# Optimization experiments

Hardware: AMD Instinct MI355X
Metric: run time of the kernel (lower is better)

The kernel has to match this reference:

```python
import jax, jax.numpy as jnp
import numpy as np

N_NODES = 50000
N_EDGES = 400000
C = 32            # channels per irrep (scalars and l=1 vectors)
N_BASIS = 8
HID = 64          # radial MLP hidden dim
N_LAYERS = 2
N_SPECIES = 86
N_GRAPHS = 64
R_MAX = 5.0
EPS = 1e-5


def setup_inputs() -> dict:
    key = jax.random.key(0)
    ks = jax.random.split(key, 16)
    species = jax.random.randint(ks[0], (N_NODES,), 0, N_SPECIES)
    pos = jax.random.normal(ks[1], (N_NODES, 3), jnp.float32)
    edge_index = jax.random.randint(ks[2], (2, N_EDGES), 0, N_NODES)
    batch = jnp.sort(jax.random.randint(ks[3], (N_NODES,), 0, N_GRAPHS))

    emb = jax.random.normal(ks[4], (N_SPECIES, C), jnp.float32) * 0.1
    freqs = jnp.arange(1, N_BASIS + 1, dtype=jnp.float32) * jnp.pi / R_MAX  # trainable Bessel freqs
    rW1 = jax.random.normal(ks[5], (N_LAYERS, N_BASIS, HID), jnp.float32) / np.sqrt(N_BASIS)
    rb1 = jnp.zeros((N_LAYERS, HID), jnp.float32)
    rW2 = jax.random.normal(ks[6], (N_LAYERS, HID, HID), jnp.float32) / np.sqrt(HID)
    rb2 = jnp.zeros((N_LAYERS, HID), jnp.float32)
    rW3 = jax.random.normal(ks[7], (N_LAYERS, HID, 4 * C), jnp.float32) / np.sqrt(HID)
    rb3 = jnp.zeros((N_LAYERS, 4 * C), jnp.float32)
    Wss = jax.random.normal(ks[8], (N_LAYERS, C, C), jnp.float32) / np.sqrt(C)
    bss = jnp.zeros((N_LAYERS, C), jnp.float32)
    Wvv = jax.random.normal(ks[9], (N_LAYERS, C, C), jnp.float32) / np.sqrt(C)
    bn_gs = jnp.ones((N_LAYERS, C), jnp.float32)
    bn_bs = jnp.zeros((N_LAYERS, C), jnp.float32)
    bn_gv = jnp.ones((N_LAYERS, C), jnp.float32)
    W_out = jax.random.normal(ks[10], (C, 1), jnp.float32) / np.sqrt(C)
    b_out = jnp.zeros((1,), jnp.float32)
    atom_ref = jnp.zeros((N_SPECIES, 1), jnp.float32)  # AtomRef init zeros
    return dict(species=species, pos=pos, edge_index=edge_index, batch=batch,
                emb=emb, freqs=freqs, rW1=rW1, rb1=rb1, rW2=rW2, rb2=rb2,
                rW3=rW3, rb3=rb3, Wss=Wss, bss=bss, Wvv=Wvv,
                bn_gs=bn_gs, bn_bs=bn_bs, bn_gv=bn_gv,
                W_out=W_out, b_out=b_out, atom_ref=atom_ref)


def _bessel_basis(dist, freqs):
    # basis = sin(f*r)/r with smooth polynomial cutoff (as in BesselRadialBasis.forward)
    d = jnp.clip(dist, 0.0)
    basis = jnp.sin(freqs[None, :] * d[:, None]) / jnp.clip(d, 1e-6)[:, None]
    x = jnp.clip(d / R_MAX, 0.0, 1.0)
    cut = 1.0 - 6.0 * x ** 5 + 15.0 * x ** 4 - 10.0 * x ** 3
    cut = jnp.where(d <= R_MAX, cut, 0.0)
    return basis * cut[:, None]


def _forward(species, pos, edge_index, batch, emb, freqs, rW1, rb1, rW2, rb2,
             rW3, rb3, Wss, bss, Wvv, bn_gs, bn_bs, bn_gv, W_out, b_out, atom_ref):
    src, dst = edge_index[0], edge_index[1]
    vec = pos[dst] - pos[src]                      # (E,3) edge vectors
    dist = jnp.sqrt(jnp.sum(vec * vec, axis=-1))   # (E,)
    basis = _bessel_basis(dist, freqs)             # (E,NB)
    Y1 = vec / jnp.clip(dist, 1e-9)[:, None]       # (E,3) l=1 spherical harmonics (unit dir)

    s = emb[species]                               # (N,C) scalar features
    v = jnp.zeros((s.shape[0], C, 3), s.dtype)     # (N,C,3) l=1 features

    for l in range(N_LAYERS):
        # radial MLP -> per-edge channel-wise tensor-product weights (4 paths x C)
        h = jax.nn.silu(basis @ rW1[l] + rb1[l])
        h = jax.nn.silu(h @ rW2[l] + rb2[l])
        w = h @ rW3[l] + rb3[l]                    # (E,4C)
        w1, w2, w3, w4 = jnp.split(w, 4, axis=-1)  # each (E,C)

        xs = s[src]                                # (E,C)   gather
        xv = v[src]                                # (E,C,3) gather
        # TP paths: s*Y0 -> scalar; (v.Y1) -> gate scalar; s*Y1 -> vector; v*Y0 -> vector
        m_sf = w1 * xs                                               # (E,C)
        m_sg = w2 * jnp.einsum('ecd,ed->ec', xv, Y1)                 # (E,C)
        m_v = w3[..., None] * xs[..., None] * Y1[:, None, :] + w4[..., None] * xv  # (E,C,3)

        agg_sf = jax.ops.segment_sum(m_sf, dst, num_segments=N_NODES)
        agg_sg = jax.ops.segment_sum(m_sg, dst, num_segments=N_NODES)
        agg_v = jax.ops.segment_sum(m_v, dst, num_segments=N_NODES)

        # gated nonlinearity: silu on scalars, sigmoid gate on vectors
        s_new = jax.nn.silu(agg_sf)
        v_new = jax.nn.sigmoid(agg_sg)[..., None] * agg_v

        # self-interaction (equivariant linear mixing over channels)
        s_new = s_new @ Wss[l] + bss[l]
        v_new = jnp.einsum('ncd,cm->nmd', v_new, Wvv[l])

        # e3nn-style batch norm: standardize scalars; norm-normalize vectors
        mu = jnp.mean(s_new, axis=0)
        var = jnp.mean((s_new - mu) ** 2, axis=0)
        s_new = (s_new - mu) / jnp.sqrt(var + EPS) * bn_gs[l] + bn_bs[l]
        vnorm2 = jnp.mean(jnp.sum(v_new * v_new, axis=-1), axis=0) / 3.0  # per-channel, /(2l+1)
        v_new = v_new / jnp.sqrt(vnorm2 + EPS)[None, :, None] * bn_gv[l][None, :, None]

        # residual (irreps match)
        s = s + s_new
        v = v + v_new

    node_e = s @ W_out + b_out                                       # (N,1)
    graph_e = jax.ops.segment_sum(node_e, batch, num_segments=N_GRAPHS)
    ref_e = jax.ops.segment_sum(atom_ref[species], batch, num_segments=N_GRAPHS)
    return graph_e + ref_e                                           # (B,1)


def reference(species, pos, edge_index, batch, emb, freqs, rW1, rb1, rW2, rb2,
              rW3, rb3, Wss, bss, Wvv, bn_gs, bn_bs, bn_gv, W_out, b_out, atom_ref):
    return _forward(species, pos, edge_index, batch, emb, freqs, rW1, rb1, rW2, rb2,
                    rW3, rb3, Wss, bss, Wvv, bn_gs, bn_bs, bn_gv, W_out, b_out, atom_ref)
```

## Files before the change

### kernel.cpp

```cpp
#include <hip/hip_runtime.h>
#include <math.h>

#define N_NODES 50000
#define N_EDGES 400000
#define C 32
#define NB 8
#define HID 64
#define NL 2
#define NG 64
#define RMAXF 5.0f
#define EPSF 1e-5f
#define TBL 4096
#define BN_BLOCKS 512
#define NBLK_N ((N_NODES + 255) / 256)

__device__ __forceinline__ float silu_f(float x) { return x / (1.0f + __expf(-x)); }
__device__ __forceinline__ float sigmoid_f(float x) { return 1.0f / (1.0f + __expf(-x)); }
__device__ __forceinline__ void atomAddF(float* p, float val) {
  __hip_atomic_fetch_add(p, val, __ATOMIC_RELAXED, __HIP_MEMORY_SCOPE_AGENT);
}
__device__ __forceinline__ void atomAddD(double* p, double val) {
  __hip_atomic_fetch_add(p, val, __ATOMIC_RELAXED, __HIP_MEMORY_SCOPE_AGENT);
}
__device__ __forceinline__ unsigned short bf16_rne(float f) {
  unsigned u = __float_as_uint(f);
  return (unsigned short)((u + 0x7FFFu + ((u >> 16) & 1u)) >> 16);
}
__device__ __forceinline__ float bfu(unsigned short u) {
  return __uint_as_float(((unsigned)u) << 16);
}

__global__ __launch_bounds__(256) void k_edge_geom(
    const float* __restrict__ pos, const int* __restrict__ ei,
    const float* __restrict__ freqs,
    float* __restrict__ basis, float* __restrict__ Y1)
{
  int e = blockIdx.x * 256 + threadIdx.x;
  if (e >= N_EDGES) return;
  int s = ei[e], d = ei[N_EDGES + e];
  float vx = pos[d*3+0] - pos[s*3+0];
  float vy = pos[d*3+1] - pos[s*3+1];
  float vz = pos[d*3+2] - pos[s*3+2];
  float dist = sqrtf(vx*vx + vy*vy + vz*vz);
  float invd = 1.0f / fmaxf(dist, 1e-9f);
  Y1[e*3+0] = vx*invd; Y1[e*3+1] = vy*invd; Y1[e*3+2] = vz*invd;
  float x = fminf(fmaxf(dist * (1.0f/RMAXF), 0.0f), 1.0f);
  float x2 = x*x, x3 = x2*x;
  float cut = 1.0f - x3 * (10.0f - 15.0f*x + 6.0f*x2);
  if (dist > RMAXF) cut = 0.0f;
  float rinv = cut / fmaxf(dist, 1e-6f);
  #pragma unroll
  for (int k = 0; k < NB; k++)
    basis[e*NB + k] = sinf(freqs[k] * dist) * rinv;
}

__global__ __launch_bounds__(256) void k_node_init(
    const int* __restrict__ species, const float* __restrict__ emb,
    float* __restrict__ s, unsigned short* __restrict__ s_bf)
{
  int i = blockIdx.x * 256 + threadIdx.x;
  if (i >= N_NODES * C) return;
  int n = i >> 5, c = i & 31;
  float x = emb[species[n]*C + c];
  s[i] = x;
  s_bf[i] = bf16_rne(x);
}

__global__ __launch_bounds__(256) void k_hist(const int* __restrict__ ei, int* __restrict__ counts)
{
  int e = blockIdx.x * 256 + threadIdx.x;
  if (e >= N_EDGES) return;
  atomicAdd(&counts[ei[N_EDGES + e]], 1);
}

__global__ __launch_bounds__(256) void k_scanA(const int* __restrict__ counts, int* __restrict__ bsum)
{
  __shared__ int sh[256];
  int i = blockIdx.x * 256 + threadIdx.x;
  int x = (i < N_NODES) ? counts[i] : 0;
  sh[threadIdx.x] = x;
  __syncthreads();
  for (int off = 128; off > 0; off >>= 1) {
    if (threadIdx.x < off) sh[threadIdx.x] += sh[threadIdx.x + off];
    __syncthreads();
  }
  if (threadIdx.x == 0) bsum[blockIdx.x] = sh[0];
}

__global__ __launch_bounds__(256) void k_scanB(int* __restrict__ bsum)
{
  __shared__ int sh[256];
  int tid = threadIdx.x;
  int x = (tid < NBLK_N) ? bsum[tid] : 0;
  sh[tid] = x;
  __syncthreads();
  for (int off = 1; off < 256; off <<= 1) {
    int y = (tid >= off) ? sh[tid - off] : 0;
    __syncthreads();
    sh[tid] += y;
    __syncthreads();
  }
  if (tid < NBLK_N) bsum[tid] = sh[tid] - x;
}

__global__ __launch_bounds__(256) void k_scanC(const int* __restrict__ counts,
                                               const int* __restrict__ bsum,
                                               int* __restrict__ row_start)
{
  __shared__ int sh[256];
  int i = blockIdx.x * 256 + threadIdx.x;
  int x = (i < N_NODES) ? counts[i] : 0;
  sh[threadIdx.x] = x;
  __syncthreads();
  for (int off = 1; off < 256; off <<= 1) {
    int y = (threadIdx.x >= off) ? sh[threadIdx.x - off] : 0;
    __syncthreads();
    sh[threadIdx.x] += y;
    __syncthreads();
  }
  if (i < N_NODES) row_start[i] = bsum[blockIdx.x] + sh[threadIdx.x] - x;
}

__global__ __launch_bounds__(256) void k_geom_scatter(
    const float* __restrict__ pos, const int* __restrict__ ei,
    const int* __restrict__ row_start, int* __restrict__ cursor,
    int* __restrict__ srcs, float* __restrict__ Y1s, float* __restrict__ dist_s)
{
  int e = blockIdx.x * 256 + threadIdx.x;
  if (e >= N_EDGES) return;
  int s = ei[e], d = ei[N_EDGES + e];
  float vx = pos[d*3+0] - pos[s*3+0];
  float vy = pos[d*3+1] - pos[s*3+1];
  float vz = pos[d*3+2] - pos[s*3+2];
  float dist = sqrtf(vx*vx + vy*vy + vz*vz);
  float invd = 1.0f / fmaxf(dist, 1e-9f);
  int p = row_start[d] + atomicAdd(&cursor[d], 1);
  srcs[p] = s;
  dist_s[p] = dist;
  Y1s[p*3+0] = vx*invd;
  Y1s[p*3+1] = vy*invd;
  Y1s[p*3+2] = vz*invd;
}

__global__ __launch_bounds__(256) void k_table_h(
    const float* __restrict__ freqs,
    const float* __restrict__ rW1, const float* __restrict__ rb1,
    const float* __restrict__ rW2, const float* __restrict__ rb2,
    float* __restrict__ h2tab)
{
  int idx = blockIdx.x * 256 + threadIdx.x;
  if (idx >= NL * TBL) return;
  int l = idx / TBL, i = idx - l * TBL;
  float d = (float)i * (RMAXF / (float)(TBL - 1));
  float x = fminf(fmaxf(d * (1.0f/RMAXF), 0.0f), 1.0f);
  float x2 = x*x, x3 = x2*x;
  float cut = 1.0f - x3 * (10.0f - 15.0f*x + 6.0f*x2);
  float rinv = cut / fmaxf(d, 1e-6f);
  float bas[NB];
  #pragma unroll
  for (int k = 0; k < NB; k++) bas[k] = sinf(freqs[k] * d) * rinv;

  const float* W1 = rW1 + l*NB*HID;
  const float* B1 = rb1 + l*HID;
  const float* W2 = rW2 + l*HID*HID;
  const float* B2 = rb2 + l*HID;

  float h2[HID];
  #pragma unroll
  for (int j = 0; j < HID; j++) h2[j] = B2[j];
  #pragma unroll 2
  for (int k = 0; k < HID; k++) {
    float t = B1[k];
    #pragma unroll
    for (int b = 0; b < NB; b++) t = fmaf(bas[b], W1[b*HID + k], t);
    float h1k = silu_f(t);
    const float* r = W2 + k*HID;
    #pragma unroll
    for (int j = 0; j < HID; j++) h2[j] = fmaf(h1k, r[j], h2[j]);
  }
  float* out = h2tab + (size_t)idx * HID;
  #pragma unroll
  for (int j = 0; j < HID; j++) out[j] = silu_f(h2[j]);
}

__global__ __launch_bounds__(256) void k_table_w(
    const float* __restrict__ h2tab,
    const float* __restrict__ rW3, const float* __restrict__ rb3,
    float* __restrict__ wtab)
{
  int idx = blockIdx.x * 256 + threadIdx.x;
  if (idx >= NL * TBL * 16) return;
  int chunk = idx & 15;
  int row   = idx >> 4;
  int l     = row / TBL;
  const float* h2 = h2tab + (size_t)row * HID;
  const float* W3 = rW3 + l*HID*4*C + chunk*8;
  const float* B3 = rb3 + l*4*C + chunk*8;
  float a[8];
  #pragma unroll
  for (int ci = 0; ci < 8; ci++) a[ci] = B3[ci];
  #pragma unroll 4
  for (int k = 0; k < HID; k++) {
    float h = h2[k];
    #pragma unroll
    for (int ci = 0; ci < 8; ci++) a[ci] = fmaf(h, W3[k*4*C + ci], a[ci]);
  }
  float* out = wtab + (size_t)row * 128 + chunk*8;
  #pragma unroll
  for (int ci = 0; ci < 8; ci++) out[ci] = a[ci];
}

__global__ __launch_bounds__(256) void k_agg_update(
    const float* __restrict__ tb,
    const float* __restrict__ dist_s, const float* __restrict__ Y1s,
    const int* __restrict__ srcs,
    const int* __restrict__ row_start, const int* __restrict__ counts,
    const unsigned short* __restrict__ s_bf, const unsigned short* __restrict__ v_bf,
    const float* __restrict__ Wss, const float* __restrict__ bss,
    const float* __restrict__ Wvv,
    float* __restrict__ s_new, float* __restrict__ v_new)
{
  int t = blockIdx.x * 256 + threadIdx.x;
  int n = t >> 5;
  int c = t & 31;

  const float SCALE = (float)(TBL - 1) / RMAXF;
  float asf = 0.0f, asg = 0.0f, av0 = 0.0f, av1 = 0.0f, av2 = 0.0f;
  int beg = row_start[n], cnt = counts[n];

  int i = 0;
  for (; i + 1 < cnt; i += 2) {
    int pA = beg + i, pB = beg + i + 1;
    float dA = dist_s[pA],  dB = dist_s[pB];
    int srcA = srcs[pA],    srcB = srcs[pB];
    float yA0 = Y1s[pA*3+0], yA1 = Y1s[pA*3+1], yA2 = Y1s[pA*3+2];
    float yB0 = Y1s[pB*3+0], yB1 = Y1s[pB*3+1], yB2 = Y1s[pB*3+2];

    float tsA = fminf(dA, RMAXF) * SCALE;
    int t0A = (int)tsA; t0A = t0A > TBL-2 ? TBL-2 : t0A;
    float frA = tsA - (float)t0A;
    float tsB = fminf(dB, RMAXF) * SCALE;
    int t0B = (int)tsB; t0B = t0B > TBL-2 ? TBL-2 : t0B;
    float frB = tsB - (float)t0B;

    const float* rA0 = tb + (size_t)t0A * 128 + c;
    const float* rA1 = rA0 + 128;
    const float* rB0 = tb + (size_t)t0B * 128 + c;
    const float* rB1 = rB0 + 128;

    float a00 = rA0[0],  a01 = rA1[0];
    float a10 = rA0[32], a11 = rA1[32];
    float a20 = rA0[64], a21 = rA1[64];
    float a30 = rA0[96], a31 = rA1[96];
    float b00 = rB0[0],  b01 = rB1[0];
    float b10 = rB0[32], b11 = rB1[32];
    float b20 = rB0[64], b21 = rB1[64];
    float b30 = rB0[96], b31 = rB1[96];

    float xsA = bfu(s_bf[srcA*C + c]);
    const unsigned short* vpA = v_bf + (size_t)(srcA*C + c)*3;
    float xvA0 = bfu(vpA[0]), xvA1 = bfu(vpA[1]), xvA2 = bfu(vpA[2]);
    float xsB = bfu(s_bf[srcB*C + c]);
    const unsigned short* vpB = v_bf + (size_t)(srcB*C + c)*3;
    float xvB0 = bfu(vpB[0]), xvB1 = bfu(vpB[1]), xvB2 = bfu(vpB[2]);

    float w1A = fmaf(frA, a01-a00, a00);
    float w2A = fmaf(frA, a11-a10, a10);
    float w3A = fmaf(frA, a21-a20, a20);
    float w4A = fmaf(frA, a31-a30, a30);
    asf = fmaf(w1A, xsA, asf);
    asg = fmaf(w2A, xvA0*yA0 + xvA1*yA1 + xvA2*yA2, asg);
    float w3xsA = w3A * xsA;
    av0 += fmaf(w3xsA, yA0, w4A*xvA0);
    av1 += fmaf(w3xsA, yA1, w4A*xvA1);
    av2 += fmaf(w3xsA, yA2, w4A*xvA2);

    float w1B = fmaf(frB, b01-b00, b00);
    float w2B = fmaf(frB, b11-b10, b10);
    float w3B = fmaf(frB, b21-b20, b20);
    float w4B = fmaf(frB, b31-b30, b30);
    asf = fmaf(w1B, xsB, asf);
    asg = fmaf(w2B, xvB0*yB0 + xvB1*yB1 + xvB2*yB2, asg);
    float w3xsB = w3B * xsB;
    av0 += fmaf(w3xsB, yB0, w4B*xvB0);
    av1 += fmaf(w3xsB, yB1, w4B*xvB1);
    av2 += fmaf(w3xsB, yB2, w4B*xvB2);
  }
  if (i < cnt) {
    int p = beg + i;
    float d  = dist_s[p];
    int src = srcs[p];
    float y0 = Y1s[p*3+0], y1 = Y1s[p*3+1], y2 = Y1s[p*3+2];
    float ts = fminf(d, RMAXF) * SCALE;
    int   t0 = (int)ts; t0 = t0 > TBL-2 ? TBL-2 : t0;
    float fr = ts - (float)t0;
    const float* r0 = tb + (size_t)t0 * 128 + c;
    const float* r1 = r0 + 128;
    float w1 = fmaf(fr, r1[0]  - r0[0],  r0[0]);
    float w2 = fmaf(fr, r1[32] - r0[32], r0[32]);
    float w3 = fmaf(fr, r1[64] - r0[64], r0[64]);
    float w4 = fmaf(fr, r1[96] - r0[96], r0[96]);
    float xs = bfu(s_bf[src*C + c]);
    const unsigned short* vp = v_bf + (size_t)(src*C + c)*3;
    float xv0 = bfu(vp[0]), xv1 = bfu(vp[1]), xv2 = bfu(vp[2]);
    asf = fmaf(w1, xs, asf);
    asg = fmaf(w2, xv0*y0 + xv1*y1 + xv2*y2, asg);
    float w3xs = w3 * xs;
    av0 += fmaf(w3xs, y0, w4*xv0);
    av1 += fmaf(w3xs, y1, w4*xv1);
    av2 += fmaf(w3xs, y2, w4*xv2);
  }

  float sgv  = silu_f(asf);
  float gate = sigmoid_f(asg);
  float vg0 = gate*av0, vg1 = gate*av1, vg2 = gate*av2;

  float sn = bss[c];
  float vm0 = 0.0f, vm1 = 0.0f, vm2 = 0.0f;
  #pragma unroll
  for (int k = 0; k < C; k++) {
    float a  = __shfl(sgv, k, 32);
    sn = fmaf(a, Wss[k*C + c], sn);
    float wv = Wvv[k*C + c];
    vm0 = fmaf(__shfl(vg0, k, 32), wv, vm0);
    vm1 = fmaf(__shfl(vg1, k, 32), wv, vm1);
    vm2 = fmaf(__shfl(vg2, k, 32), wv, vm2);
  }

  s_new[n*C + c] = sn;
  float* vo = v_new + (size_t)(n*C + c)*3;
  vo[0] = vm0; vo[1] = vm1; vo[2] = vm2;
}

__global__ __launch_bounds__(256) void k_bn_stats(
    const float* __restrict__ s_new, const float* __restrict__ v_new,
    double* __restrict__ bn_sums)
{
  __shared__ float lacc[3*C];
  if (threadIdx.x < 3*C) lacc[threadIdx.x] = 0.0f;
  __syncthreads();
  int c = threadIdx.x & 31;
  float r1 = 0.0f, r2 = 0.0f, r3 = 0.0f;
  const int NC = N_NODES * C;
  for (int i = blockIdx.x * 256 + threadIdx.x; i < NC; i += BN_BLOCKS * 256) {
    float sn = s_new[i];
    const float* vp = v_new + (size_t)i * 3;
    r1 += sn;
    r2 += sn * sn;
    r3 += vp[0]*vp[0] + vp[1]*vp[1] + vp[2]*vp[2];
  }
  atomicAdd(&lacc[c],       r1);
  atomicAdd(&lacc[C + c],   r2);
  atomicAdd(&lacc[2*C + c], r3);
  __syncthreads();
  if (threadIdx.x < 3*C) atomAddD(&bn_sums[threadIdx.x], (double)lacc[threadIdx.x]);
}

__global__ __launch_bounds__(256) void k_apply(
    const float* __restrict__ s_new, const float* __restrict__ v_new,
    const double* __restrict__ bn_sums,
    const float* __restrict__ gs, const float* __restrict__ gv,
    const float* __restrict__ bn_bs,
    float* __restrict__ s, float* __restrict__ v,
    unsigned short* __restrict__ s_bf, unsigned short* __restrict__ v_bf)
{
  int i = blockIdx.x * 256 + threadIdx.x;
  if (i >= N_NODES * C) return;
  int c = i & 31;
  double S1 = bn_sums[c], S2 = bn_sums[C + c], VN = bn_sums[2*C + c];
  float mu  = (float)(S1 / (double)N_NODES);
  float var = (float)(S2 / (double)N_NODES) - mu*mu;
  float vn2 = (float)(VN / (3.0 * (double)N_NODES));
  float ssc = gs[c] / sqrtf(var + EPSF);
  float vsc = gv[c] / sqrtf(vn2 + EPSF);

  float sv = s[i] + (s_new[i] - mu) * ssc + bn_bs[c];
  s[i] = sv;
  s_bf[i] = bf16_rne(sv);
  float* vp = v + (size_t)i*3;
  const float* vn = v_new + (size_t)i*3;
  unsigned short* vb = v_bf + (size_t)i*3;
  #pragma unroll
  for (int d = 0; d < 3; d++) {
    float vv = vp[d] + vn[d] * vsc;
    vp[d] = vv;
    vb[d] = bf16_rne(vv);
  }
}

__global__ __launch_bounds__(256) void k_readout(
    const float* __restrict__ s, const int* __restrict__ species,
    const int* __restrict__ batch,
    const float* __restrict__ W_out, const float* __restrict__ b_out,
    const float* __restrict__ atom_ref, float* __restrict__ out)
{
  __shared__ float acc[NG];
  if (threadIdx.x < NG) acc[threadIdx.x] = 0.0f;
  __syncthreads();
  int n = blockIdx.x * 256 + threadIdx.x;
  if (n < N_NODES) {
    float e = b_out[0] + atom_ref[species[n]];
    #pragma unroll
    for (int c = 0; c < C; c++) e = fmaf(s[n*C + c], W_out[c], e);
    atomicAdd(&acc[batch[n]], e);
  }
  __syncthreads();
  if (threadIdx.x < NG) {
    float a = acc[threadIdx.x];
    if (a != 0.0f) atomAddF(&out[threadIdx.x], a);
  }
}

__global__ __launch_bounds__(256) void k_edge_msg_fb(
    const float* __restrict__ basis, const float* __restrict__ Y1,
    const int* __restrict__ ei,
    const float* __restrict__ s, const float* __restrict__ v,
    const float* __restrict__ rW1, const float* __restrict__ rb1,
    const float* __restrict__ rW2, const float* __restrict__ rb2,
    const float* __restrict__ rW3, const float* __restrict__ rb3,
    float* __restrict__ agg_sf, float* __restrict__ agg_sg, float* __restrict__ agg_v)
{
  int e = blockIdx.x * 256 + threadIdx.x;
  if (e >= N_EDGES) return;
  int src = ei[e], dst = ei[N_EDGES + e];
  const float4 b0 = *(const float4*)(basis + (size_t)e*NB);
  const float4 b1 = *(const float4*)(basis + (size_t)e*NB + 4);
  float bas[NB] = {b0.x, b0.y, b0.z, b0.w, b1.x, b1.y, b1.z, b1.w};
  float h2[HID];
  #pragma unroll
  for (int j = 0; j < HID; j++) h2[j] = rb2[j];
  #pragma unroll 2
  for (int k = 0; k < HID; k++) {
    float t = rb1[k];
    #pragma unroll
    for (int b = 0; b < NB; b++) t = fmaf(bas[b], rW1[b*HID + k], t);
    float h1k = silu_f(t);
    const float* r = rW2 + k*HID;
    #pragma unroll
    for (int j = 0; j < HID; j++) h2[j] = fmaf(h1k, r[j], h2[j]);
  }
  #pragma unroll
  for (int j = 0; j < HID; j++) h2[j] = silu_f(h2[j]);
  float y0 = Y1[e*3+0], y1 = Y1[e*3+1], y2 = Y1[e*3+2];
  #pragma unroll 1
  for (int cb = 0; cb < 16; cb++) {
    float a[8];
    #pragma unroll
    for (int ci = 0; ci < 8; ci++) a[ci] = rb3[cb*8 + ci];
    #pragma unroll
    for (int k = 0; k < HID; k++) {
      float h = h2[k];
      #pragma unroll
      for (int ci = 0; ci < 8; ci++) a[ci] = fmaf(h, rW3[k*4*C + cb*8 + ci], a[ci]);
    }
    #pragma unroll
    for (int ci = 0; ci < 8; ci++) {
      int o = cb*8 + ci;
      int path = o >> 5;
      int c = o & 31;
      float xs = s[src*C + c];
      const float* vp = v + (size_t)(src*C + c)*3;
      float xv0 = vp[0], xv1 = vp[1], xv2 = vp[2];
      if (path == 0) {
        atomAddF(&agg_sf[dst*C + c], a[ci] * xs);
      } else if (path == 1) {
        atomAddF(&agg_sg[dst*C + c], a[ci] * (xv0*y0 + xv1*y1 + xv2*y2));
      } else if (path == 2) {
        float w3xs = a[ci] * xs;
        float* ap = agg_v + (size_t)(dst*C + c)*3;
        atomAddF(ap+0, w3xs*y0); atomAddF(ap+1, w3xs*y1); atomAddF(ap+2, w3xs*y2);
      } else {
        float* ap = agg_v + (size_t)(dst*C + c)*3;
        atomAddF(ap+0, a[ci]*xv0); atomAddF(ap+1, a[ci]*xv1); atomAddF(ap+2, a[ci]*xv2);
      }
    }
  }
}

__global__ __launch_bounds__(256) void k_node_update_fb(
    const float* __restrict__ agg_sf, const float* __restrict__ agg_sg,
    const float* __restrict__ agg_v,
    const float* __restrict__ Wss, const float* __restrict__ bss,
    const float* __restrict__ Wvv,
    float* __restrict__ s_new, float* __restrict__ v_new,
    double* __restrict__ bn_sums)
{
  __shared__ float lacc[3*C];
  int t = blockIdx.x * 256 + threadIdx.x;
  int n = t >> 5;
  int c = t & 31;
  if (threadIdx.x < 3*C) lacc[threadIdx.x] = 0.0f;
  __syncthreads();
  float asf = agg_sf[n*C + c];
  float asg = agg_sg[n*C + c];
  const float* ap = agg_v + (size_t)(n*C + c)*3;
  float av0 = ap[0], av1 = ap[1], av2 = ap[2];
  float sgv = silu_f(asf);
  float gate = sigmoid_f(asg);
  float vg0 = gate*av0, vg1 = gate*av1, vg2 = gate*av2;
  float sn = bss[c];
  float vm0 = 0.0f, vm1 = 0.0f, vm2 = 0.0f;
  #pragma unroll
  for (int k = 0; k < C; k++) {
    float a  = __shfl(sgv, k, 32);
    sn = fmaf(a, Wss[k*C + c], sn);
    float wv = Wvv[k*C + c];
    vm0 = fmaf(__shfl(vg0, k, 32), wv, vm0);
    vm1 = fmaf(__shfl(vg1, k, 32), wv, vm1);
    vm2 = fmaf(__shfl(vg2, k, 32), wv, vm2);
  }
  s_new[n*C + c] = sn;
  float* vo = v_new + (size_t)(n*C + c)*3;
  vo[0] = vm0; vo[1] = vm1; vo[2] = vm2;
  float vn2 = vm0*vm0 + vm1*vm1 + vm2*vm2;
  atomicAdd(&lacc[c], sn);
  atomicAdd(&lacc[C + c], sn*sn);
  atomicAdd(&lacc[2*C + c], vn2);
  __syncthreads();
  if (threadIdx.x < 3*C) atomAddD(&bn_sums[threadIdx.x], (double)lacc[threadIdx.x]);
}

__global__ void k_bn_scales_fb(const double* __restrict__ bn_sums,
                               const float* __restrict__ gs, const float* __restrict__ gv,
                               float* __restrict__ scales)
{
  int m = threadIdx.x;
  if (m >= C) return;
  double S1 = bn_sums[m], S2 = bn_sums[C + m], VN = bn_sums[2*C + m];
  double mu  = S1 / (double)N_NODES;
  double var = S2 / (double)N_NODES - mu*mu;
  double vn2 = VN / (3.0 * (double)N_NODES);
  scales[m]       = (float)mu;
  scales[C + m]   = gs[m] / sqrtf((float)var + EPSF);
  scales[2*C + m] = gv[m] / sqrtf((float)vn2 + EPSF);
}

__global__ __launch_bounds__(256) void k_apply_fb(
    const float* __restrict__ s_new, const float* __restrict__ v_new,
    const float* __restrict__ scales, const float* __restrict__ bn_bs,
    float* __restrict__ s, float* __restrict__ v)
{
  int i = blockIdx.x * 256 + threadIdx.x;
  if (i >= N_NODES * C) return;
  int c = i & 31;
  s[i] += (s_new[i] - scales[c]) * scales[C + c] + bn_bs[c];
  float vs = scales[2*C + c];
  v[(size_t)i*3+0] += v_new[(size_t)i*3+0] * vs;
  v[(size_t)i*3+1] += v_new[(size_t)i*3+1] * vs;
  v[(size_t)i*3+2] += v_new[(size_t)i*3+2] * vs;
}

extern "C" void kernel_launch(void* const* d_in, const int* in_sizes, int n_in,
                              void* d_out, int out_size, void* d_ws, size_t ws_size,
                              hipStream_t stream)
{
  const int*   species  = (const int*)  d_in[0];
  const float* pos      = (const float*)d_in[1];
  const int*   ei       = (const int*)  d_in[2];
  const int*   batch    = (const int*)  d_in[3];
  const float* emb      = (const float*)d_in[4];
  const float* freqs    = (const float*)d_in[5];
  const float* rW1      = (const float*)d_in[6];
  const float* rb1      = (const float*)d_in[7];
  const float* rW2      = (const float*)d_in[8];
  const float* rb2      = (const float*)d_in[9];
  const float* rW3      = (const float*)d_in[10];
  const float* rb3      = (const float*)d_in[11];
  const float* Wss      = (const float*)d_in[12];
  const float* bss      = (const float*)d_in[13];
  const float* Wvv      = (const float*)d_in[14];
  const float* bn_gs    = (const float*)d_in[15];
  const float* bn_bs    = (const float*)d_in[16];
  const float* bn_gv    = (const float*)d_in[17];
  const float* W_out    = (const float*)d_in[18];
  const float* b_out    = (const float*)d_in[19];
  const float* atom_ref = (const float*)d_in[20];

  float* ws = (float*)d_ws;
  size_t off = 0;
  float* basis  = ws + off; off += (size_t)N_EDGES * NB;
  float* Y1     = ws + off; off += (size_t)N_EDGES * 3;
  float* s      = ws + off; off += (size_t)N_NODES * C;
  float* v      = ws + off; off += (size_t)N_NODES * C * 3;
  float* s_new  = ws + off; off += (size_t)N_NODES * C;
  float* v_new  = ws + off; off += (size_t)N_NODES * C * 3;
  double* bn_sums = (double*)(ws + off); off += 192;
  float* scales = ws + off; off += 96;

  size_t ra = off;
  float* Y1s      = ws + ra;            ra += (size_t)N_EDGES * 3;
  float* dist_s   = ws + ra;            ra += (size_t)N_EDGES;
  int*   srcs     = (int*)(ws + ra);    ra += N_EDGES;
  int*   counts   = (int*)(ws + ra);    ra += N_NODES;
  int*   row_start= (int*)(ws + ra);    ra += N_NODES;
  int*   cursor   = (int*)(ws + ra);    ra += N_NODES;
  int*   bsum     = (int*)(ws + ra);    ra += 256;
  float* h2tab    = ws + ra;            ra += (size_t)NL * TBL * HID;
  float* wtab     = ws + ra;            ra += (size_t)NL * TBL * 128;
  unsigned short* s_bf = (unsigned short*)(ws + ra); ra += (size_t)N_NODES * C / 2;
  unsigned short* v_bf = (unsigned short*)(ws + ra); ra += (size_t)N_NODES * C * 3 / 2;
  size_t req_sorted = ra * 4;

  size_t rb = off;
  float* agg_sf = ws + rb; rb += (size_t)N_NODES * C;
  float* agg_sg = ws + rb; rb += (size_t)N_NODES * C;
  float* agg_v  = ws + rb; rb += (size_t)N_NODES * C * 3;

  dim3 b256(256);
  const int gE  = (N_EDGES + 255) / 256;
  const int gNC = (N_NODES * C + 255) / 256;
  const int gN  = (N_NODES + 255) / 256;

  hipMemsetAsync(v, 0, (size_t)N_NODES * C * 3 * sizeof(float), stream);

  if (ws_size >= req_sorted) {
    hipMemsetAsync(v_bf, 0, (size_t)N_NODES * C * 3 * sizeof(unsigned short), stream);
    hipMemsetAsync(counts, 0, N_NODES * sizeof(int), stream);
    hipMemsetAsync(cursor, 0, N_NODES * sizeof(int), stream);
    k_node_init<<<gNC, b256, 0, stream>>>(species, emb, s, s_bf);
    k_hist<<<gE, b256, 0, stream>>>(ei, counts);
    k_scanA<<<NBLK_N, b256, 0, stream>>>(counts, bsum);
    k_scanB<<<1, b256, 0, stream>>>(bsum);
    k_scanC<<<NBLK_N, b256, 0, stream>>>(counts, bsum, row_start);
    k_geom_scatter<<<gE, b256, 0, stream>>>(pos, ei, row_start, cursor,
                                            srcs, Y1s, dist_s);
    k_table_h<<<(NL*TBL)/256, b256, 0, stream>>>(freqs, rW1, rb1, rW2, rb2, h2tab);
    k_table_w<<<(NL*TBL*16)/256, b256, 0, stream>>>(h2tab, rW3, rb3, wtab);

    for (int l = 0; l < NL; l++) {
      hipMemsetAsync(bn_sums, 0, 96 * sizeof(double), stream);
      k_agg_update<<<(N_NODES*C)/256, b256, 0, stream>>>(
          wtab + (size_t)l * TBL * 128, dist_s, Y1s, srcs,
          row_start, counts, s_bf, v_bf, Wss + l*C*C, bss + l*C, Wvv + l*C*C,
          s_new, v_new);
      k_bn_stats<<<BN_BLOCKS, b256, 0, stream>>>(s_new, v_new, bn_sums);
      k_apply<<<gNC, b256, 0, stream>>>(s_new, v_new, bn_sums,
          bn_gs + l*C, bn_gv + l*C, bn_bs + l*C, s, v, s_bf, v_bf);
    }
  } else {
    k_node_init<<<gNC, b256, 0, stream>>>(species, emb, s, (unsigned short*)(ws + off));
    k_edge_geom<<<gE, b256, 0, stream>>>(pos, ei, freqs, basis, Y1);
    for (int l = 0; l < NL; l++) {
      hipMemsetAsync(agg_sf, 0, (size_t)N_NODES * 5 * C * sizeof(float), stream);
      hipMemsetAsync(bn_sums, 0, 96 * sizeof(double), stream);
      k_edge_msg_fb<<<gE, b256, 0, stream>>>(basis, Y1, ei, s, v,
          rW1 + l*NB*HID, rb1 + l*HID, rW2 + l*HID*HID, rb2 + l*HID,
          rW3 + l*HID*4*C, rb3 + l*4*C, agg_sf, agg_sg, agg_v);
      k_node_update_fb<<<(N_NODES*C)/256, b256, 0, stream>>>(agg_sf, agg_sg, agg_v,
          Wss + l*C*C, bss + l*C, Wvv + l*C*C, s_new, v_new, bn_sums);
      k_bn_scales_fb<<<1, 64, 0, stream>>>(bn_sums, bn_gs + l*C, bn_gv + l*C, scales);
      k_apply_fb<<<gNC, b256, 0, stream>>>(s_new, v_new, scales, bn_bs + l*C, s, v);
    }
  }

  hipMemsetAsync(d_out, 0, NG * sizeof(float), stream);
  k_readout<<<gN, b256, 0, stream>>>(s, species, batch, W_out, b_out, atom_ref, (float*)d_out);
}
```

Measured before the change: 332.5 us.

## Pack per-edge records into 32-byte AoS and software-prefetch next edge pair

Replaces the separate sorted arrays for source index, distance and unit vector with one 8-float record per edge, written with a float4 plus one scalar store. The aggregation loop reads each record with a vector load and prefetches the next pair of records one iteration ahead. The odd tail is handled by clamping the index and zeroing the weights, which removes the separate remainder block. The aim is fewer scattered loads and better latency hiding on the gather path. In exchange the record buffer grows, since 3 of the 8 floats per edge are padding.

```diff
diff --git a/kernel.cpp b/kernel.cpp
--- a/kernel.cpp
+++ b/kernel.cpp
@@ -124,7 +124,7 @@
 __global__ __launch_bounds__(256) void k_geom_scatter(
     const float* __restrict__ pos, const int* __restrict__ ei,
     const int* __restrict__ row_start, int* __restrict__ cursor,
-    int* __restrict__ srcs, float* __restrict__ Y1s, float* __restrict__ dist_s)
+    float* __restrict__ rec)
 {
   int e = blockIdx.x * 256 + threadIdx.x;
   if (e >= N_EDGES) return;
@@ -135,11 +135,10 @@
   float dist = sqrtf(vx*vx + vy*vy + vz*vz);
   float invd = 1.0f / fmaxf(dist, 1e-9f);
   int p = row_start[d] + atomicAdd(&cursor[d], 1);
-  srcs[p] = s;
-  dist_s[p] = dist;
-  Y1s[p*3+0] = vx*invd;
-  Y1s[p*3+1] = vy*invd;
-  Y1s[p*3+2] = vz*invd;
+  float* rp = rec + (size_t)p * 8;
+  float4 r0; r0.x = dist; r0.y = __int_as_float(s); r0.z = vx*invd; r0.w = vy*invd;
+  *(float4*)rp = r0;
+  rp[4] = vz*invd;
 }
 
 __global__ __launch_bounds__(256) void k_table_h(
@@ -212,8 +211,7 @@
 
 __global__ __launch_bounds__(256) void k_agg_update(
     const float* __restrict__ tb,
-    const float* __restrict__ dist_s, const float* __restrict__ Y1s,
-    const int* __restrict__ srcs,
+    const float* __restrict__ rec,
     const int* __restrict__ row_start, const int* __restrict__ counts,
     const unsigned short* __restrict__ s_bf, const unsigned short* __restrict__ v_bf,
     const float* __restrict__ Wss, const float* __restrict__ bss,
@@ -228,87 +226,72 @@
   float asf = 0.0f, asg = 0.0f, av0 = 0.0f, av1 = 0.0f, av2 = 0.0f;
   int beg = row_start[n], cnt = counts[n];
 
-  int i = 0;
-  for (; i + 1 < cnt; i += 2) {
-    int pA = beg + i, pB = beg + i + 1;
-    float dA = dist_s[pA],  dB = dist_s[pB];
-    int srcA = srcs[pA],    srcB = srcs[pB];
-    float yA0 = Y1s[pA*3+0], yA1 = Y1s[pA*3+1], yA2 = Y1s[pA*3+2];
-    float yB0 = Y1s[pB*3+0], yB1 = Y1s[pB*3+1], yB2 = Y1s[pB*3+2];
-
-    float tsA = fminf(dA, RMAXF) * SCALE;
-    int t0A = (int)tsA; t0A = t0A > TBL-2 ? TBL-2 : t0A;
-    float frA = tsA - (float)t0A;
-    float tsB = fminf(dB, RMAXF) * SCALE;
-    int t0B = (int)tsB; t0B = t0B > TBL-2 ? TBL-2 : t0B;
-    float frB = tsB - (float)t0B;
-
-    const float* rA0 = tb + (size_t)t0A * 128 + c;
-    const float* rA1 = rA0 + 128;
-    const float* rB0 = tb + (size_t)t0B * 128 + c;
-    const float* rB1 = rB0 + 128;
-
-    float a00 = rA0[0],  a01 = rA1[0];
-    float a10 = rA0[32], a11 = rA1[32];
-    float a20 = rA0[64], a21 = rA1[64];
-    float a30 = rA0[96], a31 = rA1[96];
-    float b00 = rB0[0],  b01 = rB1[0];
-    float b10 = rB0[32], b11 = rB1[32];
-    float b20 = rB0[64], b21 = rB1[64];
-    float b30 = rB0[96], b31 = rB1[96];
-
-    float xsA = bfu(s_bf[srcA*C + c]);
-    const unsigned short* vpA = v_bf + (size_t)(srcA*C + c)*3;
-    float xvA0 = bfu(vpA[0]), xvA1 = bfu(vpA[1]), xvA2 = bfu(vpA[2]);
-    float xsB = bfu(s_bf[srcB*C + c]);
-    const unsigned short* vpB = v_bf + (size_t)(srcB*C + c)*3;
-    float xvB0 = bfu(vpB[0]), xvB1 = bfu(vpB[1]), xvB2 = bfu(vpB[2]);
-
-    float w1A = fmaf(frA, a01-a00, a00);
-    float w2A = fmaf(frA, a11-a10, a10);
-    float w3A = fmaf(frA, a21-a20, a20);
-    float w4A = fmaf(frA, a31-a30, a30);
-    asf = fmaf(w1A, xsA, asf);
-    asg = fmaf(w2A, xvA0*yA0 + xvA1*yA1 + xvA2*yA2, asg);
-    float w3xsA = w3A * xsA;
-    av0 += fmaf(w3xsA, yA0, w4A*xvA0);
-    av1 += fmaf(w3xsA, yA1, w4A*xvA1);
-    av2 += fmaf(w3xsA, yA2, w4A*xvA2);
-
-    float w1B = fmaf(frB, b01-b00, b00);
-    float w2B = fmaf(frB, b11-b10, b10);
-    float w3B = fmaf(frB, b21-b20, b20);
-    float w4B = fmaf(frB, b31-b30, b30);
-    asf = fmaf(w1B, xsB, asf);
-    asg = fmaf(w2B, xvB0*yB0 + xvB1*yB1 + xvB2*yB2, asg);
-    float w3xsB = w3B * xsB;
-    av0 += fmaf(w3xsB, yB0, w4B*xvB0);
-    av1 += fmaf(w3xsB, yB1, w4B*xvB1);
-    av2 += fmaf(w3xsB, yB2, w4B*xvB2);
-  }
-  if (i < cnt) {
-    int p = beg + i;
-    float d  = dist_s[p];
-    int src = srcs[p];
-    float y0 = Y1s[p*3+0], y1 = Y1s[p*3+1], y2 = Y1s[p*3+2];
-    float ts = fminf(d, RMAXF) * SCALE;
-    int   t0 = (int)ts; t0 = t0 > TBL-2 ? TBL-2 : t0;
-    float fr = ts - (float)t0;
-    const float* r0 = tb + (size_t)t0 * 128 + c;
-    const float* r1 = r0 + 128;
-    float w1 = fmaf(fr, r1[0]  - r0[0],  r0[0]);
-    float w2 = fmaf(fr, r1[32] - r0[32], r0[32]);
-    float w3 = fmaf(fr, r1[64] - r0[64], r0[64]);
-    float w4 = fmaf(fr, r1[96] - r0[96], r0[96]);
-    float xs = bfu(s_bf[src*C + c]);
-    const unsigned short* vp = v_bf + (size_t)(src*C + c)*3;
-    float xv0 = bfu(vp[0]), xv1 = bfu(vp[1]), xv2 = bfu(vp[2]);
-    asf = fmaf(w1, xs, asf);
-    asg = fmaf(w2, xv0*y0 + xv1*y1 + xv2*y2, asg);
-    float w3xs = w3 * xs;
-    av0 += fmaf(w3xs, y0, w4*xv0);
-    av1 += fmaf(w3xs, y1, w4*xv1);
-    av2 += fmaf(w3xs, y2, w4*xv2);
+  if (cnt > 0) {
+    int last = beg + cnt - 1;
+    int pA = beg, pB = (beg + 1 < last) ? beg + 1 : last;
+    float4 rA = *(const float4*)(rec + (size_t)pA * 8);
+    float  zA = rec[(size_t)pA * 8 + 4];
+    float4 rB = *(const float4*)(rec + (size_t)pB * 8);
+    float  zB = rec[(size_t)pB * 8 + 4];
+
+    for (int i = 0; i < cnt; i += 2) {
+      int pA2 = beg + i + 2; pA2 = pA2 < last ? pA2 : last;
+      int pB2 = beg + i + 3; pB2 = pB2 < last ? pB2 : last;
+      float4 rA_n = *(const float4*)(rec + (size_t)pA2 * 8);
+      float  zA_n = rec[(size_t)pA2 * 8 + 4];
+      float4 rB_n = *(const float4*)(rec + (size_t)pB2 * 8);
+      float  zB_n = rec[(size_t)pB2 * 8 + 4];
+
+      float validB = (i + 1 < cnt) ? 1.0f : 0.0f;
+      float dA = rA.x;  int srcA = __float_as_int(rA.y);
+      float yA0 = rA.z, yA1 = rA.w, yA2 = zA;
+      float dB = rB.x;  int srcB = __float_as_int(rB.y);
+      float yB0 = rB.z, yB1 = rB.w, yB2 = zB;
+
+      float xsA = bfu(s_bf[srcA*C + c]);
+      const unsigned short* vpA = v_bf + (size_t)(srcA*C + c)*3;
+      float xvA0 = bfu(vpA[0]), xvA1 = bfu(vpA[1]), xvA2 = bfu(vpA[2]);
+      float xsB = bfu(s_bf[srcB*C + c]);
+      const unsigned short* vpB = v_bf + (size_t)(srcB*C + c)*3;
+      float xvB0 = bfu(vpB[0]), xvB1 = bfu(vpB[1]), xvB2 = bfu(vpB[2]);
+
+      float tsA = fminf(dA, RMAXF) * SCALE;
+      int t0A = (int)tsA; t0A = t0A > TBL-2 ? TBL-2 : t0A;
+      float frA = tsA - (float)t0A;
+      float tsB = fminf(dB, RMAXF) * SCALE;
+      int t0B = (int)tsB; t0B = t0B > TBL-2 ? TBL-2 : t0B;
+      float frB = tsB - (float)t0B;
+
+      const float* rtA0 = tb + (size_t)t0A * 128 + c;
+      const float* rtA1 = rtA0 + 128;
+      const float* rtB0 = tb + (size_t)t0B * 128 + c;
+      const float* rtB1 = rtB0 + 128;
+
+      float w1A = fmaf(frA, rtA1[0]  - rtA0[0],  rtA0[0]);
+      float w2A = fmaf(frA, rtA1[32] - rtA0[32], rtA0[32]);
+      float w3A = fmaf(frA, rtA1[64] - rtA0[64], rtA0[64]);
+      float w4A = fmaf(frA, rtA1[96] - rtA0[96], rtA0[96]);
+      float w1B = validB * fmaf(frB, rtB1[0]  - rtB0[0],  rtB0[0]);
+      float w2B = validB * fmaf(frB, rtB1[32] - rtB0[32], rtB0[32]);
+      float w3B = validB * fmaf(frB, rtB1[64] - rtB0[64], rtB0[64]);
+      float w4B = validB * fmaf(frB, rtB1[96] - rtB0[96], rtB0[96]);
+
+      asf = fmaf(w1A, xsA, asf);
+      asg = fmaf(w2A, xvA0*yA0 + xvA1*yA1 + xvA2*yA2, asg);
+      float w3xsA = w3A * xsA;
+      av0 += fmaf(w3xsA, yA0, w4A*xvA0);
+      av1 += fmaf(w3xsA, yA1, w4A*xvA1);
+      av2 += fmaf(w3xsA, yA2, w4A*xvA2);
+
+      asf = fmaf(w1B, xsB, asf);
+      asg = fmaf(w2B, xvB0*yB0 + xvB1*yB1 + xvB2*yB2, asg);
+      float w3xsB = w3B * xsB;
+      av0 += fmaf(w3xsB, yB0, w4B*xvB0);
+      av1 += fmaf(w3xsB, yB1, w4B*xvB1);
+      av2 += fmaf(w3xsB, yB2, w4B*xvB2);
+
+      rA = rA_n; zA = zA_n; rB = rB_n; zB = zB_n;
+    }
   }
 
   float sgv  = silu_f(asf);
@@ -588,9 +571,7 @@
   float* scales = ws + off; off += 96;
 
   size_t ra = off;
-  float* Y1s      = ws + ra;            ra += (size_t)N_EDGES * 3;
-  float* dist_s   = ws + ra;            ra += (size_t)N_EDGES;
-  int*   srcs     = (int*)(ws + ra);    ra += N_EDGES;
+  float* rec      = ws + ra;            ra += (size_t)N_EDGES * 8;
   int*   counts   = (int*)(ws + ra);    ra += N_NODES;
   int*   row_start= (int*)(ws + ra);    ra += N_NODES;
   int*   cursor   = (int*)(ws + ra);    ra += N_NODES;
@@ -622,15 +603,14 @@
     k_scanA<<<NBLK_N, b256, 0, stream>>>(counts, bsum);
     k_scanB<<<1, b256, 0, stream>>>(bsum);
     k_scanC<<<NBLK_N, b256, 0, stream>>>(counts, bsum, row_start);
-    k_geom_scatter<<<gE, b256, 0, stream>>>(pos, ei, row_start, cursor,
-                                            srcs, Y1s, dist_s);
+    k_geom_scatter<<<gE, b256, 0, stream>>>(pos, ei, row_start, cursor, rec);
     k_table_h<<<(NL*TBL)/256, b256, 0, stream>>>(freqs, rW1, rb1, rW2, rb2, h2tab);
     k_table_w<<<(NL*TBL*16)/256, b256, 0, stream>>>(h2tab, rW3, rb3, wtab);
 
     for (int l = 0; l < NL; l++) {
       hipMemsetAsync(bn_sums, 0, 96 * sizeof(double), stream);
       k_agg_update<<<(N_NODES*C)/256, b256, 0, stream>>>(
-          wtab + (size_t)l * TBL * 128, dist_s, Y1s, srcs,
+          wtab + (size_t)l * TBL * 128, rec,
           row_start, counts, s_bf, v_bf, Wss + l*C*C, bss + l*C, Wvv + l*C*C,
           s_new, v_new);
       k_bn_stats<<<BN_BLOCKS, b256, 0, stream>>>(s_new, v_new, bn_sums);
```

Result: faster. 321.2 us (-3.4%).
